# Kernel tuning notes

Measured on AMD Instinct MI355X. Metric: run time of the kernel, lower is better.

The kernel has to match this reference:

```python
import jax, jax.numpy as jnp
import numpy as np
from jax import lax

K = 3  # kernel size
KK = K * K

def setup_inputs() -> dict:
    key = jax.random.key(0)
    ks = jax.random.split(key, 7)
    B, C, H, W = 8, 128, 64, 64
    ck = C * KK  # 1152
    s = 0.05
    return {
        "x":   jax.random.normal(ks[0], (B, C, H, W), jnp.float32),
        "wf":  jax.random.normal(ks[1], (ck, 1, K, K), jnp.float32) * s,
        "bf":  jax.random.normal(ks[2], (ck,), jnp.float32) * s,
        "wc1": jax.random.normal(ks[3], (ck // K, KK), jnp.float32) * s,   # groups=C: [C,3,9]
        "wc2": jax.random.normal(ks[4], (ck, K), jnp.float32) * s,         # groups=C: [C,9,3]
        "wk1": jax.random.normal(ks[5], (ck // 16, C), jnp.float32) * s,   # groups=9: [9,C//16,C]
        "wk2": jax.random.normal(ks[6], (ck, C // 16), jnp.float32) * s,   # groups=9: [9,C,C//16]
    }

def reference(x, wf, bf, wc1, wc2, wk1, wk2):
    B, C, H, W = x.shape
    ck = C * KK
    # kernel_fold: depthwise-expand conv, groups=C, each channel -> 9 channels (c,k order)
    xf = lax.conv_general_dilated(
        x, wf, window_strides=(1, 1), padding=[(1, 1), (1, 1)],
        feature_group_count=C, dimension_numbers=("NCHW", "OIHW", "NCHW"))
    xf = xf + bf[None, :, None, None]              # [B, 9C, H, W]
    # global average pool
    y = jnp.mean(xf, axis=(2, 3))                  # [B, 9C] in (c,k) order
    yck = y.reshape(B, C, KK)                      # [B, C, 9]
    # fc_c branch: grouped 1x1 convs over the 9 kernel taps per channel, then shuffle to (k,c)
    hc = jax.nn.relu(jnp.einsum("bcn,con->bco", yck, wc1.reshape(C, K, KK)))
    ac = jax.nn.sigmoid(jnp.einsum("bco,cno->bcn", hc, wc2.reshape(C, KK, K)))
    ac = ac.transpose(0, 2, 1)                     # ChannelShuffle -> [B, 9, C]
    # fc_k branch: shuffle first to (k,c), grouped 1x1 convs over C channels per kernel tap
    yk = yck.transpose(0, 2, 1)                    # [B, 9, C]
    hk = jax.nn.relu(jnp.einsum("bgc,goc->bgo", yk, wk1.reshape(KK, C // 16, C)))
    ak = jax.nn.sigmoid(jnp.einsum("bgo,gco->bgc", hk, wk2.reshape(KK, C, C // 16)))
    # dual SE gate (flat channel order (k,c), multiplied against xf in (c,k) order, as in torch)
    gate = (ac * ak).reshape(B, ck)                # [B, 9C]
    attn = jnp.broadcast_to(gate[:, :, None, None], xf.shape)
    return xf * gate[:, :, None, None], attn
```

## Files before the change

### kernel.cpp

```cpp
#include <hip/hip_runtime.h>
#include <hip/hip_bf16.h>

static constexpr int Bn  = 8;
static constexpr int Cn  = 128;
static constexpr int KKn = 9;
static constexpr int CKn = Cn * KKn;
static constexpr int PIX = 64 * 64;
static constexpr long long OUT_HALF = (long long)Bn * CKn * PIX;

__global__ __launch_bounds__(256) void k_stats(const float* __restrict__ x,
                                               const float* __restrict__ wf,
                                               const float* __restrict__ bf,
                                               float* __restrict__ yck) {
    const int bc = blockIdx.x;
    const float* xp = x + (size_t)bc * PIX;
    const int t = threadIdx.x;

    float tot = 0.f, r0 = 0.f, r63 = 0.f, c0 = 0.f, c63 = 0.f;
#pragma unroll
    for (int i = 0; i < 4; ++i) {
        int p = (i * 256 + t) * 4;
        float4 v = *reinterpret_cast<const float4*>(xp + p);
        int h = p >> 6;
        int w = p & 63;
        float s = v.x + v.y + v.z + v.w;
        tot += s;
        if (h == 0)  r0  += s;
        if (h == 63) r63 += s;
        if (w == 0)  c0  += v.x;
        if (w == 60) c63 += v.w;
    }

    const int lane = t & 63, wid = t >> 6;
#pragma unroll
    for (int off = 32; off; off >>= 1) {
        tot += __shfl_down(tot, off, 64);
        r0  += __shfl_down(r0,  off, 64);
        r63 += __shfl_down(r63, off, 64);
        c0  += __shfl_down(c0,  off, 64);
        c63 += __shfl_down(c63, off, 64);
    }
    __shared__ float part[4][5];
    __shared__ float S[9];
    if (lane == 0) {
        part[wid][0] = tot; part[wid][1] = r0; part[wid][2] = r63;
        part[wid][3] = c0;  part[wid][4] = c63;
    }
    __syncthreads();
    if (t == 0) {
        float T  = part[0][0] + part[1][0] + part[2][0] + part[3][0];
        float R0 = part[0][1] + part[1][1] + part[2][1] + part[3][1];
        float RB = part[0][2] + part[1][2] + part[2][2] + part[3][2];
        float CL = part[0][3] + part[1][3] + part[2][3] + part[3][3];
        float CR = part[0][4] + part[1][4] + part[2][4] + part[3][4];
        float x00 = xp[0], x0R = xp[63], xB0 = xp[63 * 64], xBR = xp[4095];
#pragma unroll
        for (int dh = -1; dh <= 1; ++dh) {
#pragma unroll
            for (int dw = -1; dw <= 1; ++dw) {
                float rex = (dh == -1) ? RB : (dh == 1 ? R0 : 0.f);
                float cex = (dw == -1) ? CR : (dw == 1 ? CL : 0.f);
                float crn = 0.f;
                if (dh != 0 && dw != 0) {
                    crn = (dh == -1) ? ((dw == -1) ? xBR : xB0)
                                     : ((dw == -1) ? x0R : x00);
                }
                S[(dh + 1) * 3 + (dw + 1)] = T - rex - cex + crn;
            }
        }
    }
    __syncthreads();
    if (t < 9) {
        int o = (bc & 127) * 9 + t;
        const float* wp = wf + o * 9;
        float s = 0.f;
#pragma unroll
        for (int j = 0; j < 9; ++j) s = fmaf(wp[j], S[j], s);
        yck[(size_t)bc * 9 + t] = bf[o] + s * (1.f / 4096.f);
    }
}

__global__ __launch_bounds__(128) void k_gate(const float* __restrict__ yck,
                                              const float* __restrict__ wc1,
                                              const float* __restrict__ wc2,
                                              const float* __restrict__ wk1,
                                              const float* __restrict__ wk2,
                                              float* __restrict__ gate) {
    const int b = blockIdx.x;
    const int c = threadIdx.x;

    __shared__ float ylds[Cn][KKn];
    __shared__ float aclds[Cn][KKn];
    __shared__ float hks[KKn][8];

    const float* yp = yck + ((size_t)b * Cn + c) * KKn;
    float yv[KKn];
#pragma unroll
    for (int k = 0; k < 9; ++k) { yv[k] = yp[k]; ylds[c][k] = yv[k]; }

    float hc[3];
#pragma unroll
    for (int o = 0; o < 3; ++o) {
        float s = 0.f;
#pragma unroll
        for (int n = 0; n < 9; ++n) s = fmaf(yv[n], wc1[(c * 3 + o) * 9 + n], s);
        hc[o] = fmaxf(s, 0.f);
    }
#pragma unroll
    for (int n = 0; n < 9; ++n) {
        float s = 0.f;
#pragma unroll
        for (int o = 0; o < 3; ++o) s = fmaf(hc[o], wc2[(c * 9 + n) * 3 + o], s);
        aclds[c][n] = 1.f / (1.f + expf(-s));
    }
    __syncthreads();

    if (c < 72) {
        int g = c / 8, o = c % 8;
        float s = 0.f;
        for (int cc = 0; cc < Cn; ++cc) s = fmaf(ylds[cc][g], wk1[(g * 8 + o) * Cn + cc], s);
        hks[g][o] = fmaxf(s, 0.f);
    }
    __syncthreads();

#pragma unroll
    for (int g = 0; g < 9; ++g) {
        float s = 0.f;
#pragma unroll
        for (int o = 0; o < 8; ++o) s = fmaf(hks[g][o], wk2[(g * Cn + c) * 8 + o], s);
        float ak = 1.f / (1.f + expf(-s));
        gate[(size_t)b * CKn + g * Cn + c] = aclds[c][g] * ak;
    }
}

__global__ __launch_bounds__(256) void k_out(const float* __restrict__ x,
                                             const float* __restrict__ wf,
                                             const float* __restrict__ bf,
                                             const float* __restrict__ gate,
                                             float* __restrict__ out0,
                                             float* __restrict__ out1) {
    const int bc = blockIdx.x;
    const int b = bc >> 7;
    const int c = bc & 127;
    const float* xp = x + (size_t)bc * PIX;
    const int t = threadIdx.x;

    __shared__ float wsh[KKn][KKn];
    __shared__ float bsh[KKn];
    __shared__ float gsh[KKn];
    if (t < 81) wsh[t / 9][t % 9] = wf[(size_t)(c * 9) * 9 + t];
    if (t < 9) {
        bsh[t] = bf[c * 9 + t];
        gsh[t] = gate[(size_t)b * CKn + c * 9 + t];
    }
    __syncthreads();

#pragma unroll
    for (int it = 0; it < 4; ++it) {
        int p = it * 1024 + t * 4;
        int h = p >> 6;
        int w = p & 63;

        float rowv[3][6];
#pragma unroll
        for (int dh = 0; dh < 3; ++dh) {
            int hh = h + dh - 1;
            if (hh < 0 || hh > 63) {
#pragma unroll
                for (int j = 0; j < 6; ++j) rowv[dh][j] = 0.f;
            } else {
                const float* rp = xp + hh * 64 + w;
                float4 cen = *reinterpret_cast<const float4*>(rp);
                rowv[dh][1] = cen.x; rowv[dh][2] = cen.y;
                rowv[dh][3] = cen.z; rowv[dh][4] = cen.w;
                rowv[dh][0] = (w > 0)  ? rp[-1] : 0.f;
                rowv[dh][5] = (w < 60) ? rp[4]  : 0.f;
            }
        }

        size_t outBase = (size_t)bc * 9 * PIX + p;
#pragma unroll
        for (int k = 0; k < 9; ++k) {
            float acc0 = bsh[k], acc1 = bsh[k], acc2 = bsh[k], acc3 = bsh[k];
#pragma unroll
            for (int dh = 0; dh < 3; ++dh) {
#pragma unroll
                for (int dw = 0; dw < 3; ++dw) {
                    float wv = wsh[k][dh * 3 + dw];
                    acc0 = fmaf(rowv[dh][0 + dw], wv, acc0);
                    acc1 = fmaf(rowv[dh][1 + dw], wv, acc1);
                    acc2 = fmaf(rowv[dh][2 + dw], wv, acc2);
                    acc3 = fmaf(rowv[dh][3 + dw], wv, acc3);
                }
            }
            float g = gsh[k];
            float4 o0 = make_float4(acc0 * g, acc1 * g, acc2 * g, acc3 * g);
            float4 o1 = make_float4(g, g, g, g);
            *reinterpret_cast<float4*>(out0 + outBase + (size_t)k * PIX) = o0;
            *reinterpret_cast<float4*>(out1 + outBase + (size_t)k * PIX) = o1;
        }
    }
}

extern "C" void kernel_launch(void* const* d_in, const int* in_sizes, int n_in,
                              void* d_out, int out_size, void* d_ws, size_t ws_size,
                              hipStream_t stream) {
    const float* x   = (const float*)d_in[0];
    const float* wf  = (const float*)d_in[1];
    const float* bf  = (const float*)d_in[2];
    const float* wc1 = (const float*)d_in[3];
    const float* wc2 = (const float*)d_in[4];
    const float* wk1 = (const float*)d_in[5];
    const float* wk2 = (const float*)d_in[6];

    float* out0 = (float*)d_out;
    float* out1 = out0 + OUT_HALF;

    float* yck  = (float*)d_ws;
    float* gate = yck + (size_t)Bn * Cn * KKn;

    k_stats<<<Bn * Cn, 256, 0, stream>>>(x, wf, bf, yck);
    k_gate<<<Bn, 128, 0, stream>>>(yck, wc1, wc2, wk1, wk2, gate);
    k_out<<<Bn * Cn, 256, 0, stream>>>(x, wf, bf, gate, out0, out1);
}
```

Measured before the change: 68.96 us.

## Fuse stats and gate kernels via last-block atomic; widen output tiles with nontemporal stores

Merges the pooling-stats kernel and the gate MLP kernel into one launch. The last block to finish for each batch, found with an atomic counter, computes the gate, which removes one kernel launch. Separately, the output kernel now computes 8 pixels per thread and writes with nontemporal stores to cut cache pollution on the large output stream. The counter in the workspace is never reset, so the code relies on modulo-128 counting across calls.

After: 177.2 us. 2.57x slower.

```diff
diff --git a/kernel.cpp b/kernel.cpp
--- a/kernel.cpp
+++ b/kernel.cpp
@@ -1,5 +1,7 @@
 #include <hip/hip_runtime.h>
 #include <hip/hip_bf16.h>
+
+typedef float f32x4 __attribute__((ext_vector_type(4)));
 
 static constexpr int Bn  = 8;
 static constexpr int Cn  = 128;
@@ -8,11 +10,22 @@
 static constexpr int PIX = 64 * 64;
 static constexpr long long OUT_HALF = (long long)Bn * CKn * PIX;
 
-__global__ __launch_bounds__(256) void k_stats(const float* __restrict__ x,
-                                               const float* __restrict__ wf,
-                                               const float* __restrict__ bf,
-                                               float* __restrict__ yck) {
+static __device__ __forceinline__ void ntst(f32x4 v, float* p) {
+    __builtin_nontemporal_store(v, (f32x4*)p);
+}
+
+__global__ __launch_bounds__(256) void k_stats_gate(const float* __restrict__ x,
+                                                    const float* __restrict__ wf,
+                                                    const float* __restrict__ bf,
+                                                    const float* __restrict__ wc1,
+                                                    const float* __restrict__ wc2,
+                                                    const float* __restrict__ wk1,
+                                                    const float* __restrict__ wk2,
+                                                    float* __restrict__ yck,
+                                                    float* __restrict__ gate,
+                                                    unsigned* __restrict__ cnt) {
     const int bc = blockIdx.x;
+    const int b = bc >> 7;
     const float* xp = x + (size_t)bc * PIX;
     const int t = threadIdx.x;
 
@@ -77,59 +90,66 @@
 #pragma unroll
         for (int j = 0; j < 9; ++j) s = fmaf(wp[j], S[j], s);
         yck[(size_t)bc * 9 + t] = bf[o] + s * (1.f / 4096.f);
-    }
-}
-
-__global__ __launch_bounds__(128) void k_gate(const float* __restrict__ yck,
-                                              const float* __restrict__ wc1,
-                                              const float* __restrict__ wc2,
-                                              const float* __restrict__ wk1,
-                                              const float* __restrict__ wk2,
-                                              float* __restrict__ gate) {
-    const int b = blockIdx.x;
-    const int c = threadIdx.x;
+        __threadfence();
+    }
+    __syncthreads();
+
+    __shared__ int isLast;
+    if (t == 0) {
+        unsigned old = atomicAdd(&cnt[b], 1u);
+        isLast = ((old & 127u) == 127u);
+    }
+    __syncthreads();
+    if (!isLast) return;
+    __threadfence();
 
     __shared__ float ylds[Cn][KKn];
     __shared__ float aclds[Cn][KKn];
     __shared__ float hks[KKn][8];
-
-    const float* yp = yck + ((size_t)b * Cn + c) * KKn;
-    float yv[KKn];
-#pragma unroll
-    for (int k = 0; k < 9; ++k) { yv[k] = yp[k]; ylds[c][k] = yv[k]; }
-
-    float hc[3];
-#pragma unroll
-    for (int o = 0; o < 3; ++o) {
+    const float* ybase = yck + (size_t)b * CKn;
+    for (int idx = t; idx < CKn; idx += 256)
+        ylds[idx / 9][idx % 9] = ybase[idx];
+    __syncthreads();
+
+    if (t < Cn) {
+        const int c = t;
+        float yv[KKn];
+#pragma unroll
+        for (int k = 0; k < 9; ++k) yv[k] = ylds[c][k];
+        float hc[3];
+#pragma unroll
+        for (int o = 0; o < 3; ++o) {
+            float s = 0.f;
+#pragma unroll
+            for (int n = 0; n < 9; ++n) s = fmaf(yv[n], wc1[(c * 3 + o) * 9 + n], s);
+            hc[o] = fmaxf(s, 0.f);
+        }
+#pragma unroll
+        for (int n = 0; n < 9; ++n) {
+            float s = 0.f;
+#pragma unroll
+            for (int o = 0; o < 3; ++o) s = fmaf(hc[o], wc2[(c * 9 + n) * 3 + o], s);
+            aclds[c][n] = 1.f / (1.f + expf(-s));
+        }
+    } else if (t < Cn + 72) {
+        const int gg = (t - Cn) / 8, o = (t - Cn) % 8;
         float s = 0.f;
-#pragma unroll
-        for (int n = 0; n < 9; ++n) s = fmaf(yv[n], wc1[(c * 3 + o) * 9 + n], s);
-        hc[o] = fmaxf(s, 0.f);
-    }
-#pragma unroll
-    for (int n = 0; n < 9; ++n) {
-        float s = 0.f;
-#pragma unroll
-        for (int o = 0; o < 3; ++o) s = fmaf(hc[o], wc2[(c * 9 + n) * 3 + o], s);
-        aclds[c][n] = 1.f / (1.f + expf(-s));
-    }
-    __syncthreads();
-
-    if (c < 72) {
-        int g = c / 8, o = c % 8;
-        float s = 0.f;
-        for (int cc = 0; cc < Cn; ++cc) s = fmaf(ylds[cc][g], wk1[(g * 8 + o) * Cn + cc], s);
-        hks[g][o] = fmaxf(s, 0.f);
-    }
-    __syncthreads();
-
-#pragma unroll
-    for (int g = 0; g < 9; ++g) {
-        float s = 0.f;
-#pragma unroll
-        for (int o = 0; o < 8; ++o) s = fmaf(hks[g][o], wk2[(g * Cn + c) * 8 + o], s);
-        float ak = 1.f / (1.f + expf(-s));
-        gate[(size_t)b * CKn + g * Cn + c] = aclds[c][g] * ak;
+        for (int cc = 0; cc < Cn; ++cc)
+            s = fmaf(ylds[cc][gg], wk1[(gg * 8 + o) * Cn + cc], s);
+        hks[gg][o] = fmaxf(s, 0.f);
+    }
+    __syncthreads();
+
+    if (t < Cn) {
+        const int c = t;
+#pragma unroll
+        for (int g = 0; g < 9; ++g) {
+            float s = 0.f;
+#pragma unroll
+            for (int o = 0; o < 8; ++o) s = fmaf(hks[g][o], wk2[(g * Cn + c) * 8 + o], s);
+            float ak = 1.f / (1.f + expf(-s));
+            gate[(size_t)b * CKn + g * Cn + c] = aclds[c][g] * ak;
+        }
     }
 }
 
@@ -156,48 +176,55 @@
     __syncthreads();
 
 #pragma unroll
-    for (int it = 0; it < 4; ++it) {
-        int p = it * 1024 + t * 4;
-        int h = p >> 6;
-        int w = p & 63;
-
-        float rowv[3][6];
+    for (int it = 0; it < 2; ++it) {
+        const int p = (it * 256 + t) * 8;
+        const int h = p >> 6;
+        const int w = p & 63;
+
+        float rowv[3][10];
 #pragma unroll
         for (int dh = 0; dh < 3; ++dh) {
-            int hh = h + dh - 1;
+            const int hh = h + dh - 1;
             if (hh < 0 || hh > 63) {
 #pragma unroll
-                for (int j = 0; j < 6; ++j) rowv[dh][j] = 0.f;
+                for (int j = 0; j < 10; ++j) rowv[dh][j] = 0.f;
             } else {
                 const float* rp = xp + hh * 64 + w;
-                float4 cen = *reinterpret_cast<const float4*>(rp);
-                rowv[dh][1] = cen.x; rowv[dh][2] = cen.y;
-                rowv[dh][3] = cen.z; rowv[dh][4] = cen.w;
+                f32x4 a  = *reinterpret_cast<const f32x4*>(rp);
+                f32x4 b2 = *reinterpret_cast<const f32x4*>(rp + 4);
+                rowv[dh][1] = a.x; rowv[dh][2] = a.y; rowv[dh][3] = a.z; rowv[dh][4] = a.w;
+                rowv[dh][5] = b2.x; rowv[dh][6] = b2.y; rowv[dh][7] = b2.z; rowv[dh][8] = b2.w;
                 rowv[dh][0] = (w > 0)  ? rp[-1] : 0.f;
-                rowv[dh][5] = (w < 60) ? rp[4]  : 0.f;
+                rowv[dh][9] = (w < 56) ? rp[8]  : 0.f;
             }
         }
 
-        size_t outBase = (size_t)bc * 9 * PIX + p;
+        const size_t outBase = (size_t)bc * 9 * PIX + p;
 #pragma unroll
         for (int k = 0; k < 9; ++k) {
-            float acc0 = bsh[k], acc1 = bsh[k], acc2 = bsh[k], acc3 = bsh[k];
+            float acc[8];
+#pragma unroll
+            for (int j = 0; j < 8; ++j) acc[j] = bsh[k];
 #pragma unroll
             for (int dh = 0; dh < 3; ++dh) {
 #pragma unroll
                 for (int dw = 0; dw < 3; ++dw) {
-                    float wv = wsh[k][dh * 3 + dw];
-                    acc0 = fmaf(rowv[dh][0 + dw], wv, acc0);
-                    acc1 = fmaf(rowv[dh][1 + dw], wv, acc1);
-                    acc2 = fmaf(rowv[dh][2 + dw], wv, acc2);
-                    acc3 = fmaf(rowv[dh][3 + dw], wv, acc3);
+                    const float wv = wsh[k][dh * 3 + dw];
+#pragma unroll
+                    for (int j = 0; j < 8; ++j)
+                        acc[j] = fmaf(rowv[dh][j + dw], wv, acc[j]);
                 }
             }
-            float g = gsh[k];
-            float4 o0 = make_float4(acc0 * g, acc1 * g, acc2 * g, acc3 * g);
-            float4 o1 = make_float4(g, g, g, g);
-            *reinterpret_cast<float4*>(out0 + outBase + (size_t)k * PIX) = o0;
-            *reinterpret_cast<float4*>(out1 + outBase + (size_t)k * PIX) = o1;
+            const float g = gsh[k];
+            f32x4 lo = { acc[0] * g, acc[1] * g, acc[2] * g, acc[3] * g };
+            f32x4 hi = { acc[4] * g, acc[5] * g, acc[6] * g, acc[7] * g };
+            f32x4 gv = { g, g, g, g };
+            float* o0 = out0 + outBase + (size_t)k * PIX;
+            float* o1 = out1 + outBase + (size_t)k * PIX;
+            ntst(lo, o0);
+            ntst(hi, o0 + 4);
+            ntst(gv, o1);
+            ntst(gv, o1 + 4);
         }
     }
 }
@@ -216,10 +243,11 @@
     float* out0 = (float*)d_out;
     float* out1 = out0 + OUT_HALF;
 
-    float* yck  = (float*)d_ws;
-    float* gate = yck + (size_t)Bn * Cn * KKn;
-
-    k_stats<<<Bn * Cn, 256, 0, stream>>>(x, wf, bf, yck);
-    k_gate<<<Bn, 128, 0, stream>>>(yck, wc1, wc2, wk1, wk2, gate);
+    float*    yck  = (float*)d_ws;
+    float*    gate = yck + (size_t)Bn * Cn * KKn;
+    unsigned* cnt  = (unsigned*)(gate + (size_t)Bn * CKn);
+
+    k_stats_gate<<<Bn * Cn, 256, 0, stream>>>(x, wf, bf, wc1, wc2, wk1, wk2,
+                                              yck, gate, cnt);
     k_out<<<Bn * Cn, 256, 0, stream>>>(x, wf, bf, gate, out0, out1);
 }
```
